# Performance work log

Hardware: AMD Instinct MI355X
Metric: run time of the kernel (lower is better)

Reference implementation:

```python
import jax, jax.numpy as jnp
import numpy as np

HEADS = 8
EMBED = 64
FEAT_A = 256
FEAT_B = 256


def setup_inputs() -> dict:
    key = jax.random.key(0)
    k1, k2, k3, k4, k5 = jax.random.split(key, 5)
    B, N = 2, 2048
    z_a = jax.random.normal(k1, (B, FEAT_A, N), dtype=jnp.float32)
    z_b = jax.random.normal(k2, (B, FEAT_B, N), dtype=jnp.float32)
    # Conv1d(k=1, bias=False) weights, squeezed: [out_ch, in_ch]
    W_a = jax.random.normal(k3, (HEADS * EMBED, FEAT_A), dtype=jnp.float32) * (1.0 / np.sqrt(FEAT_A))
    W_b = jax.random.normal(k4, (HEADS * EMBED, FEAT_B), dtype=jnp.float32) * (1.0 / np.sqrt(FEAT_B))
    W_c = jax.random.normal(k5, (FEAT_A, HEADS * FEAT_B), dtype=jnp.float32) * (1.0 / np.sqrt(HEADS * FEAT_B))
    return {"z_a": z_a, "z_b": z_b, "W_a": W_a, "W_b": W_b, "W_c": W_c}


def reference(z_a, z_b, W_a, W_b, W_c):
    B, Fa, Na = z_a.shape
    Fb = z_b.shape[1]
    H, E = HEADS, EMBED
    norm = 1.0 / np.sqrt(E)
    # 1x1 conv embeddings -> q, k: [B, H, E, N]
    q = jnp.einsum('of,bfn->bon', W_a, z_a).reshape(B, H, E, Na)
    k = jnp.einsum('of,bfn->bon', W_b, z_b).reshape(B, H, E, -1)
    v = z_b  # [B, Fb, K]
    # coeff_pre_softmax[b,h,q,k] = (q^T k) / sqrt(E)
    pre = jnp.einsum('bheq,bhek->bhqk', q, k) * norm
    coeff = jax.nn.softmax(pre, axis=-1)  # softmax over keys (dim=2 in torch bmm form)
    # l1 loss: mean |pre| over (q,k) per head, averaged over heads
    l1 = jnp.mean(jnp.abs(pre), axis=(1, 2, 3))  # [B]
    # feat[b,h,q,f] = coeff @ v^T
    feat = jnp.einsum('bhqk,bfk->bhqf', coeff, v)
    # combine heads: w[h] = W_c[:, h*Fb:(h+1)*Fb].T  -> [H, Fb, Fa]
    w = W_c.reshape(Fa, H, Fb).transpose(1, 2, 0)
    out = jnp.einsum('bhqf,hfo->bqo', feat, w)  # sum over heads
    return out, l1
```

## Files before the change

### kernel.cpp

```cpp
#include <hip/hip_runtime.h>
#include <hip/hip_bf16.h>


#define B_ 2
#define N_ 2048
#define F_ 256
#define H_ 8
#define E_ 64

typedef __attribute__((ext_vector_type(8))) short bf16x8;
typedef __attribute__((ext_vector_type(4))) float f32x4;

__device__ __forceinline__ unsigned short f2b(float x) {
  __hip_bfloat16 h = __float2bfloat16(x);
  return *reinterpret_cast<unsigned short*>(&h);
}

__device__ __forceinline__ unsigned short f2bt(float x) {
  union { float f; unsigned u; } c; c.f = x;
  return (unsigned short)(c.u >> 16);
}

__device__ __forceinline__ f32x4 mfma16(bf16x8 a, bf16x8 b, f32x4 c) {
  return __builtin_amdgcn_mfma_f32_16x16x32_bf16(a, b, c, 0, 0, 0);
}

__device__ __forceinline__ void async_lds16(const unsigned short* g, unsigned short* l) {
  __builtin_amdgcn_global_load_lds(
      (const __attribute__((address_space(1))) unsigned int*)g,
      (__attribute__((address_space(3))) unsigned int*)l, 16, 0, 0);
}

__global__ __launch_bounds__(256) void prep_kernel(
    const float* __restrict__ W_c, unsigned short* __restrict__ wcb,
    const float* __restrict__ W_a, const float* __restrict__ W_b,
    unsigned short* __restrict__ wab, float* __restrict__ l1acc) {
  int i = blockIdx.x * 256 + threadIdx.x;
  if (i < B_) l1acc[i] = 0.f;
  const int nwc = F_ * H_ * F_ / 4;
  const int nw = 512 * F_ / 4;
  const float* src; unsigned short* dst; int j;
  if (i < nwc) { src = W_c; dst = wcb; j = i; }
  else if (i < nwc + nw) { src = W_a; dst = wab; j = i - nwc; }
  else { j = i - nwc - nw; src = W_b; dst = wab + 512 * F_; }
  float4 v = reinterpret_cast<const float4*>(src)[j];
  unsigned long long pk =
      ((unsigned long long)f2b(v.w) << 48) | ((unsigned long long)f2b(v.z) << 32) |
      ((unsigned long long)f2b(v.y) << 16) | (unsigned long long)f2b(v.x);
  reinterpret_cast<unsigned long long*>(dst)[j] = pk;
}

__global__ __launch_bounds__(256) void fused_tp(
    const float* __restrict__ z_a, const float* __restrict__ z_b,
    const unsigned short* __restrict__ wab, unsigned short* __restrict__ vbf,
    unsigned short* __restrict__ qT, unsigned short* __restrict__ kT) {
  __shared__ unsigned int t32[64][33];
  __shared__ __align__(16) unsigned short As[32][256];

  const int tid = threadIdx.x;
  const int nt = blockIdx.x, oh = blockIdx.y, wz = blockIdx.z;
  const int b = wz & 1, which = wz >> 1;
  const float* src = (which ? z_b : z_a) + (size_t)b * F_ * N_;

  const int n4 = (tid & 7) * 4;
  const int frow = tid >> 3;
  const int n_l = tid & 31;
  const int jb = tid >> 5;

#pragma unroll
  for (int s = 0; s < 4; ++s) {
#pragma unroll
    for (int pass = 0; pass < 2; ++pass) {
      int f_l = pass * 32 + frow;
      float4 v = *reinterpret_cast<const float4*>(
          &src[(size_t)(s * 64 + f_l) * N_ + nt * 32 + n4]);
      unsigned short u0 = f2b(v.x), u1 = f2b(v.y), u2 = f2b(v.z), u3 = f2b(v.w);
      t32[f_l][n4] = u0; t32[f_l][n4 + 1] = u1;
      t32[f_l][n4 + 2] = u2; t32[f_l][n4 + 3] = u3;
      if (which && oh == 0) {
        ushort4 pk = {u0, u1, u2, u3};
        *reinterpret_cast<ushort4*>(
            &vbf[(size_t)(b * F_ + s * 64 + f_l) * 2048 + nt * 32 + n4]) = pk;
      }
    }
    __syncthreads();
    {
      int c = s * 8 + jb;
      int p = c ^ n_l;
      unsigned w0 = t32[jb * 8 + 0][n_l] | (t32[jb * 8 + 1][n_l] << 16);
      unsigned w1 = t32[jb * 8 + 2][n_l] | (t32[jb * 8 + 3][n_l] << 16);
      unsigned w2 = t32[jb * 8 + 4][n_l] | (t32[jb * 8 + 5][n_l] << 16);
      unsigned w3 = t32[jb * 8 + 6][n_l] | (t32[jb * 8 + 7][n_l] << 16);
      uint4 pk = {w0, w1, w2, w3};
      *reinterpret_cast<uint4*>(&As[n_l][p * 8]) = pk;
    }
    __syncthreads();
  }

  const int wid = tid >> 6, lane = tid & 63;
  const int quad = lane >> 4, l16 = lane & 15;
  const unsigned short* wsrc = wab + (size_t)which * 512 * F_;
  unsigned short* dst = (which ? kT : qT) + (size_t)b * N_ * 512;
  const float scale = which ? 1.f : 0.125f;
  const f32x4 zero4 = {0.f, 0.f, 0.f, 0.f};

#pragma unroll
  for (int ot = 0; ot < 4; ++ot) {
    const int o = (oh * 4 + ot) * 64 + wid * 16 + l16;
    const unsigned short* brow = wsrc + (size_t)o * F_ + quad * 8;
    f32x4 acc0 = zero4, acc1 = zero4;
#pragma unroll
    for (int kt = 0; kt < 8; ++kt) {
      bf16x8 bf = *reinterpret_cast<const bf16x8*>(brow + kt * 32);
      const int row0 = l16, row1 = 16 + l16;
      bf16x8 a0 = *reinterpret_cast<const bf16x8*>(
          &As[0][0] + row0 * 256 + ((kt * 4 + quad) ^ row0) * 8);
      bf16x8 a1 = *reinterpret_cast<const bf16x8*>(
          &As[0][0] + row1 * 256 + ((kt * 4 + quad) ^ row1) * 8);
      acc0 = mfma16(a0, bf, acc0);
      acc1 = mfma16(a1, bf, acc1);
    }
#pragma unroll
    for (int r = 0; r < 4; ++r) {
      dst[(size_t)(nt * 32 + quad * 4 + r) * 512 + o] = f2b(acc0[r] * scale);
      dst[(size_t)(nt * 32 + 16 + quad * 4 + r) * 512 + o] = f2b(acc1[r] * scale);
    }
  }
}

__global__ __launch_bounds__(256, 3) void attn_mfma(
    const unsigned short* __restrict__ qT, const unsigned short* __restrict__ kT,
    const unsigned short* __restrict__ vbf, unsigned short* __restrict__ feat,
    float* __restrict__ l1acc) {
  __shared__ __align__(16) unsigned short ks[2][32][64];
  __shared__ __align__(16) unsigned short vs[2][256][32];
  __shared__ __align__(16) unsigned short p_blk[2][64][40];
  __shared__ float lsum_sh[64];
  __shared__ float redblk[256];

  const int tid = threadIdx.x;
  const int wid = tid >> 6, lane = tid & 63;
  const int quad = lane >> 4, l16 = lane & 15;
  const int qt = blockIdx.x, h = blockIdx.y, b = blockIdx.z;

  const int kkey = wid * 8 + (lane >> 3);
  const int kchunk = (lane & 7) ^ ((kkey >> 1) & 7);
  const unsigned short* kgl =
      kT + ((size_t)(b * N_ + kkey) * 512) + h * 64 + kchunk * 8;
  const unsigned short* vgl[4];
#pragma unroll
  for (int j = 0; j < 4; ++j) {
    int f = (wid * 4 + j) * 16 + (lane >> 2);
    int c = (lane & 3) ^ ((f >> 1) & 3);
    vgl[j] = vbf + ((size_t)(b * F_ + f) * 2048) + c * 8;
  }

  const unsigned short* qrow =
      qT + (size_t)(b * N_ + qt * 64 + wid * 16 + l16) * 512 + h * 64 + quad * 8;
  bf16x8 qf0 = *reinterpret_cast<const bf16x8*>(qrow);
  bf16x8 qf1 = *reinterpret_cast<const bf16x8*>(qrow + 32);

  const int koff = ((quad ^ (l16 & 7)) * 8);
  const int voff = ((quad ^ ((l16 >> 1) & 3)) * 8);

  f32x4 acc[4][4];
  const f32x4 zero4 = {0.f, 0.f, 0.f, 0.f};
#pragma unroll
  for (int g = 0; g < 4; ++g)
#pragma unroll
    for (int t = 0; t < 4; ++t) acc[g][t] = zero4;
  float lsum[4] = {0.f, 0.f, 0.f, 0.f};
  float suml1 = 0.f;
  bf16x8 vreg[4];

  async_lds16(kgl, &ks[0][wid * 8][0]);
#pragma unroll
  for (int j = 0; j < 4; ++j) async_lds16(vgl[j], &vs[0][(wid * 4 + j) * 16][0]);
  __syncthreads();

#pragma unroll 2
  for (int kt = 0; kt < N_ / 32; ++kt) {
    const int cur = kt & 1;
    if (kt + 1 < N_ / 32) {
      async_lds16(kgl + (size_t)(kt + 1) * 32 * 512, &ks[cur ^ 1][wid * 8][0]);
#pragma unroll
      for (int j = 0; j < 4; ++j)
        async_lds16(vgl[j] + (kt + 1) * 32, &vs[cur ^ 1][(wid * 4 + j) * 16][0]);
    }

    const unsigned short* ksc = &ks[cur][0][0];
    bf16x8 kf00 = *reinterpret_cast<const bf16x8*>(ksc + (2 * l16) * 64 + koff);
    bf16x8 kf01 = *reinterpret_cast<const bf16x8*>(ksc + (2 * l16) * 64 + (koff ^ 32));
    bf16x8 kf10 = *reinterpret_cast<const bf16x8*>(ksc + (2 * l16 + 1) * 64 + koff);
    bf16x8 kf11 = *reinterpret_cast<const bf16x8*>(ksc + (2 * l16 + 1) * 64 + (koff ^ 32));

    f32x4 s0 = mfma16(qf0, kf00, zero4); s0 = mfma16(qf1, kf01, s0);
    f32x4 s1 = mfma16(qf0, kf10, zero4); s1 = mfma16(qf1, kf11, s1);

#pragma unroll
    for (int r = 0; r < 4; ++r) {
      float a0 = s0[r], a1 = s1[r];
      suml1 += fabsf(a0) + fabsf(a1);
      float p0 = __expf(a0), p1 = __expf(a1);
      lsum[r] += p0 + p1;
      unsigned pk = ((unsigned)f2bt(p1) << 16) | f2bt(p0);
      *reinterpret_cast<unsigned*>(&p_blk[cur][wid * 16 + quad * 4 + r][2 * l16]) = pk;
    }

    if (kt > 0) {
#pragma unroll
      for (int g = 0; g < 4; ++g) {
        bf16x8 pf = *reinterpret_cast<const bf16x8*>(&p_blk[cur ^ 1][g * 16 + l16][quad * 8]);
#pragma unroll
        for (int t = 0; t < 4; ++t) acc[g][t] = mfma16(pf, vreg[t], acc[g][t]);
      }
    }

    {
      const unsigned short* vsc = &vs[cur][0][0];
#pragma unroll
      for (int t = 0; t < 4; ++t) {
        int f = wid * 64 + t * 16 + l16;
        vreg[t] = *reinterpret_cast<const bf16x8*>(vsc + f * 32 + voff);
      }
    }
    __syncthreads();
  }

  {
#pragma unroll
    for (int g = 0; g < 4; ++g) {
      bf16x8 pf = *reinterpret_cast<const bf16x8*>(&p_blk[1][g * 16 + l16][quad * 8]);
#pragma unroll
      for (int t = 0; t < 4; ++t) acc[g][t] = mfma16(pf, vreg[t], acc[g][t]);
    }
  }

#pragma unroll
  for (int r = 0; r < 4; ++r) {
    float rs = lsum[r];
    rs += __shfl_xor(rs, 1);
    rs += __shfl_xor(rs, 2);
    rs += __shfl_xor(rs, 4);
    rs += __shfl_xor(rs, 8);
    if (l16 == 0) lsum_sh[wid * 16 + quad * 4 + r] = rs;
  }
  __syncthreads();

#pragma unroll
  for (int g = 0; g < 4; ++g)
#pragma unroll
    for (int r = 0; r < 4; ++r) {
      float invl = 1.f / lsum_sh[g * 16 + quad * 4 + r];
      unsigned short* fr =
          feat + (size_t)(b * N_ + qt * 64 + g * 16 + quad * 4 + r) * 2048 +
          h * 256 + wid * 64 + l16;
#pragma unroll
      for (int t = 0; t < 4; ++t) fr[t * 16] = f2b(acc[g][t][r] * invl);
    }

  redblk[tid] = suml1;
  __syncthreads();
  for (int st = 128; st > 0; st >>= 1) {
    if (tid < st) redblk[tid] += redblk[tid + st];
    __syncthreads();
  }
  if (tid == 0) atomicAdd(&l1acc[b], redblk[0]);
}

__global__ __launch_bounds__(256) void combine_mfma(
    const unsigned short* __restrict__ feat, const unsigned short* __restrict__ wcb,
    const float* __restrict__ l1acc, float* __restrict__ out) {
  __shared__ __align__(16) unsigned short As[2][64][256];

  const int tid = threadIdx.x;
  const int wid = tid >> 6, lane = tid & 63;
  const int quad = lane >> 4, l16 = lane & 15;
  const int mb = blockIdx.x, ob = blockIdx.y;

  const int srow_hi = lane >> 5;
  const int spos = lane & 31;

  const unsigned short* brow = wcb + (size_t)(ob * 64 + wid * 16 + l16) * 2048 + quad * 8;

  f32x4 acc[4];
  const f32x4 zero4 = {0.f, 0.f, 0.f, 0.f};
#pragma unroll
  for (int g = 0; g < 4; ++g) acc[g] = zero4;

#pragma unroll
  for (int i = 0; i < 8; ++i) {
    int row = wid * 16 + 2 * i + srow_hi;
    int cg = spos ^ (row & 31);
    async_lds16(feat + (size_t)(mb * 64 + row) * 2048 + cg * 8, &As[0][wid * 16 + 2 * i][0]);
  }
  __syncthreads();

  for (int ch = 0; ch < 8; ++ch) {
    const int cur = ch & 1;
    if (ch + 1 < 8) {
#pragma unroll
      for (int i = 0; i < 8; ++i) {
        int row = wid * 16 + 2 * i + srow_hi;
        int cg = spos ^ (row & 31);
        async_lds16(feat + (size_t)(mb * 64 + row) * 2048 + (ch + 1) * 256 + cg * 8,
                    &As[cur ^ 1][wid * 16 + 2 * i][0]);
      }
    }
#pragma unroll
    for (int kt = 0; kt < 8; ++kt) {
      bf16x8 bf = *reinterpret_cast<const bf16x8*>(brow + ch * 256 + kt * 32);
#pragma unroll
      for (int g = 0; g < 4; ++g) {
        int row = g * 16 + l16;
        int p = (kt * 4 + quad) ^ (row & 31);
        bf16x8 af = *reinterpret_cast<const bf16x8*>(&As[cur][0][0] + row * 256 + p * 8);
        acc[g] = mfma16(af, bf, acc[g]);
      }
    }
    __syncthreads();
  }

#pragma unroll
  for (int g = 0; g < 4; ++g)
#pragma unroll
    for (int r = 0; r < 4; ++r)
      out[(size_t)(mb * 64 + g * 16 + quad * 4 + r) * 256 + ob * 64 + wid * 16 + l16] =
          acc[g][r];

  if (mb == 0 && ob == 0 && tid < B_)
    out[(size_t)B_ * N_ * F_ + tid] = l1acc[tid] * (1.f / (float)(H_ * N_ * N_));
}

extern "C" void kernel_launch(void* const* d_in, const int* in_sizes, int n_in,
                              void* d_out, int out_size, void* d_ws, size_t ws_size,
                              hipStream_t stream) {
  const float* z_a = (const float*)d_in[0];
  const float* z_b = (const float*)d_in[1];
  const float* W_a = (const float*)d_in[2];
  const float* W_b = (const float*)d_in[3];
  const float* W_c = (const float*)d_in[4];
  float* out = (float*)d_out;

  char* ws = (char*)d_ws;
  unsigned short* qT = (unsigned short*)ws;
  unsigned short* kT = (unsigned short*)(ws + ((size_t)4 << 20));
  unsigned short* vbf = (unsigned short*)(ws + ((size_t)8 << 20));
  unsigned short* wcb = (unsigned short*)(ws + ((size_t)10 << 20));
  unsigned short* wab = (unsigned short*)(ws + ((size_t)15 << 20));
  float* l1acc = (float*)(ws + ((size_t)15 << 20) + (768 << 10));
  unsigned short* feat = (unsigned short*)(ws + ((size_t)16 << 20));

  const int nprep = F_ * H_ * F_ / 4 + 2 * (512 * F_ / 4);
  prep_kernel<<<dim3(nprep / 256), 256, 0, stream>>>(
      W_c, wcb, W_a, W_b, wab, l1acc);
  fused_tp<<<dim3(N_ / 32, 2, 4), 256, 0, stream>>>(z_a, z_b, wab, vbf, qT, kT);
  attn_mfma<<<dim3(N_ / 64, H_, B_), 256, 0, stream>>>(qT, kT, vbf, feat, l1acc);
  combine_mfma<<<dim3(B_ * N_ / 64, 4), 256, 0, stream>>>(feat, wcb, l1acc, out);
}
```

Measured before the change: 165.9 us.

## Merge four kernels into one cooperative persistent kernel with grid syncs

Result: slower. 360.8 us (+117.5%).

```diff
diff --git a/kernel.cpp b/kernel.cpp
--- a/kernel.cpp
+++ b/kernel.cpp
@@ -1,5 +1,6 @@
 #include <hip/hip_runtime.h>
 #include <hip/hip_bf16.h>
+#include <hip/hip_cooperative_groups.h>
 
 
 #define B_ 2
@@ -8,6 +9,8 @@
 #define H_ 8
 #define E_ 64
 
+namespace cg = cooperative_groups;
+
 typedef __attribute__((ext_vector_type(8))) short bf16x8;
 typedef __attribute__((ext_vector_type(4))) float f32x4;
 
@@ -31,34 +34,49 @@
       (__attribute__((address_space(3))) unsigned int*)l, 16, 0, 0);
 }
 
-__global__ __launch_bounds__(256) void prep_kernel(
+union SMem {
+  struct {
+    unsigned int t32[64][33];
+    __align__(16) unsigned short As[32][256];
+  } tp;
+  struct {
+    __align__(16) unsigned short ks[2][32][64];
+    __align__(16) unsigned short vs[2][256][32];
+    __align__(16) unsigned short p_blk[2][64][40];
+    float lsum_sh[64];
+    float redblk[256];
+  } at;
+  struct {
+    __align__(16) unsigned short As[2][32][256];
+  } cb;
+};
+
+__device__ __forceinline__ void prep_body(
+    int gtid, int nthreads,
     const float* __restrict__ W_c, unsigned short* __restrict__ wcb,
     const float* __restrict__ W_a, const float* __restrict__ W_b,
     unsigned short* __restrict__ wab, float* __restrict__ l1acc) {
-  int i = blockIdx.x * 256 + threadIdx.x;
-  if (i < B_) l1acc[i] = 0.f;
+  if (gtid < B_) l1acc[gtid] = 0.f;
   const int nwc = F_ * H_ * F_ / 4;
   const int nw = 512 * F_ / 4;
-  const float* src; unsigned short* dst; int j;
-  if (i < nwc) { src = W_c; dst = wcb; j = i; }
-  else if (i < nwc + nw) { src = W_a; dst = wab; j = i - nwc; }
-  else { j = i - nwc - nw; src = W_b; dst = wab + 512 * F_; }
-  float4 v = reinterpret_cast<const float4*>(src)[j];
-  unsigned long long pk =
-      ((unsigned long long)f2b(v.w) << 48) | ((unsigned long long)f2b(v.z) << 32) |
-      ((unsigned long long)f2b(v.y) << 16) | (unsigned long long)f2b(v.x);
-  reinterpret_cast<unsigned long long*>(dst)[j] = pk;
-}
-
-__global__ __launch_bounds__(256) void fused_tp(
+  for (int j0 = gtid; j0 < nwc + 2 * nw; j0 += nthreads) {
+    const float* src; unsigned short* dst; int j;
+    if (j0 < nwc) { src = W_c; dst = wcb; j = j0; }
+    else if (j0 < nwc + nw) { src = W_a; dst = wab; j = j0 - nwc; }
+    else { src = W_b; dst = wab + 512 * F_; j = j0 - nwc - nw; }
+    float4 v = reinterpret_cast<const float4*>(src)[j];
+    unsigned long long pk =
+        ((unsigned long long)f2b(v.w) << 48) | ((unsigned long long)f2b(v.z) << 32) |
+        ((unsigned long long)f2b(v.y) << 16) | (unsigned long long)f2b(v.x);
+    reinterpret_cast<unsigned long long*>(dst)[j] = pk;
+  }
+}
+
+__device__ __forceinline__ void tp_body(
+    SMem& sm, int tid, int nt, int oh, int wz,
     const float* __restrict__ z_a, const float* __restrict__ z_b,
     const unsigned short* __restrict__ wab, unsigned short* __restrict__ vbf,
     unsigned short* __restrict__ qT, unsigned short* __restrict__ kT) {
-  __shared__ unsigned int t32[64][33];
-  __shared__ __align__(16) unsigned short As[32][256];
-
-  const int tid = threadIdx.x;
-  const int nt = blockIdx.x, oh = blockIdx.y, wz = blockIdx.z;
   const int b = wz & 1, which = wz >> 1;
   const float* src = (which ? z_b : z_a) + (size_t)b * F_ * N_;
 
@@ -75,8 +93,8 @@
       float4 v = *reinterpret_cast<const float4*>(
           &src[(size_t)(s * 64 + f_l) * N_ + nt * 32 + n4]);
       unsigned short u0 = f2b(v.x), u1 = f2b(v.y), u2 = f2b(v.z), u3 = f2b(v.w);
-      t32[f_l][n4] = u0; t32[f_l][n4 + 1] = u1;
-      t32[f_l][n4 + 2] = u2; t32[f_l][n4 + 3] = u3;
+      sm.tp.t32[f_l][n4] = u0; sm.tp.t32[f_l][n4 + 1] = u1;
+      sm.tp.t32[f_l][n4 + 2] = u2; sm.tp.t32[f_l][n4 + 3] = u3;
       if (which && oh == 0) {
         ushort4 pk = {u0, u1, u2, u3};
         *reinterpret_cast<ushort4*>(
@@ -87,12 +105,12 @@
     {
       int c = s * 8 + jb;
       int p = c ^ n_l;
-      unsigned w0 = t32[jb * 8 + 0][n_l] | (t32[jb * 8 + 1][n_l] << 16);
-      unsigned w1 = t32[jb * 8 + 2][n_l] | (t32[jb * 8 + 3][n_l] << 16);
-      unsigned w2 = t32[jb * 8 + 4][n_l] | (t32[jb * 8 + 5][n_l] << 16);
-      unsigned w3 = t32[jb * 8 + 6][n_l] | (t32[jb * 8 + 7][n_l] << 16);
+      unsigned w0 = sm.tp.t32[jb * 8 + 0][n_l] | (sm.tp.t32[jb * 8 + 1][n_l] << 16);
+      unsigned w1 = sm.tp.t32[jb * 8 + 2][n_l] | (sm.tp.t32[jb * 8 + 3][n_l] << 16);
+      unsigned w2 = sm.tp.t32[jb * 8 + 4][n_l] | (sm.tp.t32[jb * 8 + 5][n_l] << 16);
+      unsigned w3 = sm.tp.t32[jb * 8 + 6][n_l] | (sm.tp.t32[jb * 8 + 7][n_l] << 16);
       uint4 pk = {w0, w1, w2, w3};
-      *reinterpret_cast<uint4*>(&As[n_l][p * 8]) = pk;
+      *reinterpret_cast<uint4*>(&sm.tp.As[n_l][p * 8]) = pk;
     }
     __syncthreads();
   }
@@ -114,9 +132,9 @@
       bf16x8 bf = *reinterpret_cast<const bf16x8*>(brow + kt * 32);
       const int row0 = l16, row1 = 16 + l16;
       bf16x8 a0 = *reinterpret_cast<const bf16x8*>(
-          &As[0][0] + row0 * 256 + ((kt * 4 + quad) ^ row0) * 8);
+          &sm.tp.As[0][0] + row0 * 256 + ((kt * 4 + quad) ^ row0) * 8);
       bf16x8 a1 = *reinterpret_cast<const bf16x8*>(
-          &As[0][0] + row1 * 256 + ((kt * 4 + quad) ^ row1) * 8);
+          &sm.tp.As[0][0] + row1 * 256 + ((kt * 4 + quad) ^ row1) * 8);
       acc0 = mfma16(a0, bf, acc0);
       acc1 = mfma16(a1, bf, acc1);
     }
@@ -128,20 +146,19 @@
   }
 }
 
-__global__ __launch_bounds__(256, 3) void attn_mfma(
+__device__ __forceinline__ void attn_body(
+    SMem& sm, int tid, int qt, int h, int b,
     const unsigned short* __restrict__ qT, const unsigned short* __restrict__ kT,
     const unsigned short* __restrict__ vbf, unsigned short* __restrict__ feat,
     float* __restrict__ l1acc) {
-  __shared__ __align__(16) unsigned short ks[2][32][64];
-  __shared__ __align__(16) unsigned short vs[2][256][32];
-  __shared__ __align__(16) unsigned short p_blk[2][64][40];
-  __shared__ float lsum_sh[64];
-  __shared__ float redblk[256];
-
-  const int tid = threadIdx.x;
+  unsigned short (&ks)[2][32][64] = sm.at.ks;
+  unsigned short (&vs)[2][256][32] = sm.at.vs;
+  unsigned short (&p_blk)[2][64][40] = sm.at.p_blk;
+  float (&lsum_sh)[64] = sm.at.lsum_sh;
+  float (&redblk)[256] = sm.at.redblk;
+
   const int wid = tid >> 6, lane = tid & 63;
   const int quad = lane >> 4, l16 = lane & 15;
-  const int qt = blockIdx.x, h = blockIdx.y, b = blockIdx.z;
 
   const int kkey = wid * 8 + (lane >> 3);
   const int kchunk = (lane & 7) ^ ((kkey >> 1) & 7);
@@ -268,68 +285,116 @@
   if (tid == 0) atomicAdd(&l1acc[b], redblk[0]);
 }
 
+__device__ __forceinline__ void combine_body(
+    SMem& sm, int tid, int mb, int ob,
+    const unsigned short* __restrict__ feat, const unsigned short* __restrict__ wcb,
+    const float* __restrict__ l1acc, float* __restrict__ out) {
+  const int wid = tid >> 6, lane = tid & 63;
+  const int quad = lane >> 4, l16 = lane & 15;
+
+  const int srow_hi = lane >> 5;
+  const int spos = lane & 31;
+
+  const unsigned short* brow = wcb + (size_t)(ob * 64 + wid * 16 + l16) * 2048 + quad * 8;
+
+  f32x4 acc[2];
+  const f32x4 zero4 = {0.f, 0.f, 0.f, 0.f};
+  acc[0] = zero4; acc[1] = zero4;
+
+#pragma unroll
+  for (int i = 0; i < 4; ++i) {
+    int row = wid * 8 + 2 * i + srow_hi;
+    int cg = spos ^ row;
+    async_lds16(feat + (size_t)(mb * 32 + row) * 2048 + cg * 8,
+                &sm.cb.As[0][wid * 8 + 2 * i][0]);
+  }
+  __syncthreads();
+
+  for (int ch = 0; ch < 8; ++ch) {
+    const int cur = ch & 1;
+    if (ch + 1 < 8) {
+#pragma unroll
+      for (int i = 0; i < 4; ++i) {
+        int row = wid * 8 + 2 * i + srow_hi;
+        int cg = spos ^ row;
+        async_lds16(feat + (size_t)(mb * 32 + row) * 2048 + (ch + 1) * 256 + cg * 8,
+                    &sm.cb.As[cur ^ 1][wid * 8 + 2 * i][0]);
+      }
+    }
+#pragma unroll
+    for (int kt = 0; kt < 8; ++kt) {
+      bf16x8 bf = *reinterpret_cast<const bf16x8*>(brow + ch * 256 + kt * 32);
+#pragma unroll
+      for (int g = 0; g < 2; ++g) {
+        int row = g * 16 + l16;
+        int p = (kt * 4 + quad) ^ row;
+        bf16x8 af = *reinterpret_cast<const bf16x8*>(&sm.cb.As[cur][0][0] + row * 256 + p * 8);
+        acc[g] = mfma16(af, bf, acc[g]);
+      }
+    }
+    __syncthreads();
+  }
+
+#pragma unroll
+  for (int g = 0; g < 2; ++g)
+#pragma unroll
+    for (int r = 0; r < 4; ++r)
+      out[(size_t)(mb * 32 + g * 16 + quad * 4 + r) * 256 + ob * 64 + wid * 16 + l16] =
+          acc[g][r];
+
+  if (mb == 0 && ob == 0 && tid < B_)
+    out[(size_t)B_ * N_ * F_ + tid] = l1acc[tid] * (1.f / (float)(H_ * N_ * N_));
+}
+
+__global__ __launch_bounds__(256, 2) void mega_kernel(
+    const float* __restrict__ z_a, const float* __restrict__ z_b,
+    const float* __restrict__ W_a, const float* __restrict__ W_b,
+    const float* __restrict__ W_c, float* __restrict__ out,
+    unsigned short* __restrict__ qT, unsigned short* __restrict__ kT,
+    unsigned short* __restrict__ vbf, unsigned short* __restrict__ wcb,
+    unsigned short* __restrict__ wab, float* __restrict__ l1acc,
+    unsigned short* __restrict__ feat) {
+  __shared__ SMem sm;
+  cg::grid_group grid = cg::this_grid();
+  const int bx = blockIdx.x, tid = threadIdx.x;
+
+  prep_body(bx * 256 + tid, 512 * 256, W_c, wcb, W_a, W_b, wab, l1acc);
+  grid.sync();
+  tp_body(sm, tid, bx & 63, (bx >> 6) & 1, bx >> 7, z_a, z_b, wab, vbf, qT, kT);
+  grid.sync();
+  attn_body(sm, tid, bx & 31, (bx >> 5) & 7, bx >> 8, qT, kT, vbf, feat, l1acc);
+  grid.sync();
+  combine_body(sm, tid, bx & 127, bx >> 7, feat, wcb, l1acc, out);
+}
+
+__global__ __launch_bounds__(256) void prep_kernel(
+    const float* __restrict__ W_c, unsigned short* __restrict__ wcb,
+    const float* __restrict__ W_a, const float* __restrict__ W_b,
+    unsigned short* __restrict__ wab, float* __restrict__ l1acc) {
+  prep_body(blockIdx.x * 256 + threadIdx.x, 512 * 256, W_c, wcb, W_a, W_b, wab, l1acc);
+}
+
+__global__ __launch_bounds__(256) void fused_tp(
+    const float* __restrict__ z_a, const float* __restrict__ z_b,
+    const unsigned short* __restrict__ wab, unsigned short* __restrict__ vbf,
+    unsigned short* __restrict__ qT, unsigned short* __restrict__ kT) {
+  __shared__ SMem sm;
+  tp_body(sm, threadIdx.x, blockIdx.x, blockIdx.y, blockIdx.z, z_a, z_b, wab, vbf, qT, kT);
+}
+
+__global__ __launch_bounds__(256, 3) void attn_mfma(
+    const unsigned short* __restrict__ qT, const unsigned short* __restrict__ kT,
+    const unsigned short* __restrict__ vbf, unsigned short* __restrict__ feat,
+    float* __restrict__ l1acc) {
+  __shared__ SMem sm;
+  attn_body(sm, threadIdx.x, blockIdx.x, blockIdx.y, blockIdx.z, qT, kT, vbf, feat, l1acc);
+}
+
 __global__ __launch_bounds__(256) void combine_mfma(
     const unsigned short* __restrict__ feat, const unsigned short* __restrict__ wcb,
     const float* __restrict__ l1acc, float* __restrict__ out) {
-  __shared__ __align__(16) unsigned short As[2][64][256];
-
-  const int tid = threadIdx.x;
-  const int wid = tid >> 6, lane = tid & 63;
-  const int quad = lane >> 4, l16 = lane & 15;
-  const int mb = blockIdx.x, ob = blockIdx.y;
-
-  const int srow_hi = lane >> 5;
-  const int spos = lane & 31;
-
-  const unsigned short* brow = wcb + (size_t)(ob * 64 + wid * 16 + l16) * 2048 + quad * 8;
-
-  f32x4 acc[4];
-  const f32x4 zero4 = {0.f, 0.f, 0.f, 0.f};
-#pragma unroll
-  for (int g = 0; g < 4; ++g) acc[g] = zero4;
-
-#pragma unroll
-  for (int i = 0; i < 8; ++i) {
-    int row = wid * 16 + 2 * i + srow_hi;
-    int cg = spos ^ (row & 31);
-    async_lds16(feat + (size_t)(mb * 64 + row) * 2048 + cg * 8, &As[0][wid * 16 + 2 * i][0]);
-  }
-  __syncthreads();
-
-  for (int ch = 0; ch < 8; ++ch) {
-    const int cur = ch & 1;
-    if (ch + 1 < 8) {
-#pragma unroll
-      for (int i = 0; i < 8; ++i) {
-        int row = wid * 16 + 2 * i + srow_hi;
-        int cg = spos ^ (row & 31);
-        async_lds16(feat + (size_t)(mb * 64 + row) * 2048 + (ch + 1) * 256 + cg * 8,
-                    &As[cur ^ 1][wid * 16 + 2 * i][0]);
-      }
-    }
-#pragma unroll
-    for (int kt = 0; kt < 8; ++kt) {
-      bf16x8 bf = *reinterpret_cast<const bf16x8*>(brow + ch * 256 + kt * 32);
-#pragma unroll
-      for (int g = 0; g < 4; ++g) {
-        int row = g * 16 + l16;
-        int p = (kt * 4 + quad) ^ (row & 31);
-        bf16x8 af = *reinterpret_cast<const bf16x8*>(&As[cur][0][0] + row * 256 + p * 8);
-        acc[g] = mfma16(af, bf, acc[g]);
-      }
-    }
-    __syncthreads();
-  }
-
-#pragma unroll
-  for (int g = 0; g < 4; ++g)
-#pragma unroll
-    for (int r = 0; r < 4; ++r)
-      out[(size_t)(mb * 64 + g * 16 + quad * 4 + r) * 256 + ob * 64 + wid * 16 + l16] =
-          acc[g][r];
-
-  if (mb == 0 && ob == 0 && tid < B_)
-    out[(size_t)B_ * N_ * F_ + tid] = l1acc[tid] * (1.f / (float)(H_ * N_ * N_));
+  __shared__ SMem sm;
+  combine_body(sm, threadIdx.x, blockIdx.x, blockIdx.y, feat, wcb, l1acc, out);
 }
 
 extern "C" void kernel_launch(void* const* d_in, const int* in_sizes, int n_in,
@@ -351,10 +416,16 @@
   float* l1acc = (float*)(ws + ((size_t)15 << 20) + (768 << 10));
   unsigned short* feat = (unsigned short*)(ws + ((size_t)16 << 20));
 
-  const int nprep = F_ * H_ * F_ / 4 + 2 * (512 * F_ / 4);
-  prep_kernel<<<dim3(nprep / 256), 256, 0, stream>>>(
-      W_c, wcb, W_a, W_b, wab, l1acc);
-  fused_tp<<<dim3(N_ / 32, 2, 4), 256, 0, stream>>>(z_a, z_b, wab, vbf, qT, kT);
-  attn_mfma<<<dim3(N_ / 64, H_, B_), 256, 0, stream>>>(qT, kT, vbf, feat, l1acc);
-  combine_mfma<<<dim3(B_ * N_ / 64, 4), 256, 0, stream>>>(feat, wcb, l1acc, out);
-}
+  void* args[] = {&z_a, &z_b, &W_a, &W_b, &W_c, &out,
+                  &qT, &kT, &vbf, &wcb, &wab, &l1acc, &feat};
+  hipError_t e = hipLaunchCooperativeKernel(
+      reinterpret_cast<const void*>(&mega_kernel), dim3(512), dim3(256),
+      args, 0, stream);
+  if (e != hipSuccess) {
+    (void)hipGetLastError();
+    prep_kernel<<<dim3(512), 256, 0, stream>>>(W_c, wcb, W_a, W_b, wab, l1acc);
+    fused_tp<<<dim3(N_ / 32, 2, 4), 256, 0, stream>>>(z_a, z_b, wab, vbf, qT, kT);
+    attn_mfma<<<dim3(N_ / 64, H_, B_), 256, 0, stream>>>(qT, kT, vbf, feat, l1acc);
+    combine_mfma<<<dim3(B_ * N_ / 32, 4), 256, 0, stream>>>(feat, wcb, l1acc, out);
+  }
+}
```
